# Optimization experiments

Measured on AMD Instinct MI355X. Metric: run time of the kernel, lower is better.

The kernel has to match this reference:

```python
import jax, jax.numpy as jnp
import numpy as np

B, T, P, D, H, L, C = 32, 50000, 100, 512, 16, 6, 256
SCALES = [1, 2, 4]
NS = len(SCALES)
HS = H // NS          # heads per scale = 5
KD = D // H           # key_dim = 32
N = T // P            # num_patches = 500
FF = 4 * D
EPS = 1e-3            # keras LayerNormalization default epsilon


def layernorm(x, g, b):
    m = jnp.mean(x, axis=-1, keepdims=True)
    v = jnp.var(x, axis=-1, keepdims=True)
    return (x - m) * jax.lax.rsqrt(v + EPS) * g + b


def mha(x, Wq, bq, Wk, bk, Wv, bv, Wo, bo):
    # keras MultiHeadAttention: self-attention, scale 1/sqrt(key_dim), biases on
    q = jnp.einsum('bnd,dhk->bnhk', x, Wq) + bq
    k = jnp.einsum('bnd,dhk->bnhk', x, Wk) + bk
    v = jnp.einsum('bnd,dhk->bnhk', x, Wv) + bv
    scores = jnp.einsum('bnhk,bmhk->bhnm', q, k) / jnp.sqrt(jnp.asarray(KD, x.dtype))
    p = jax.nn.softmax(scores, axis=-1)
    o = jnp.einsum('bhnm,bmhk->bnhk', p, v)
    return jnp.einsum('bnhk,hkd->bnd', o, Wo) + bo


def forward(inputs, ln_in_g, ln_in_b, patch_W, patch_b, pos_emb,
            Wq, bq, Wk, bk, Wv, bv, Wo, bo, Wc, bc,
            ln1_g, ln1_b, W1, b1, W2, b2, ln2_g, ln2_b, head_W, head_b):
    x = inputs[..., None]                       # (B, T, 1)
    x = layernorm(x, ln_in_g, ln_in_b)          # degenerate size-1 LN (faithful)
    patches = x.reshape(B, N, P)                # (B, N, P)
    h = patches @ patch_W + patch_b + pos_emb   # (B, N, D)
    for l in range(L):
        outs = []
        for si, s in enumerate(SCALES):
            if s > 1:
                pooled = h.reshape(B, N // s, s, D).mean(axis=2)  # SAME avg_pool1d (N % s == 0)
            else:
                pooled = h
            a = mha(pooled, Wq[l, si], bq[l, si], Wk[l, si], bk[l, si],
                    Wv[l, si], bv[l, si], Wo[l, si], bo[l, si])
            if s > 1:
                a = jnp.repeat(a, s, axis=1)[:, :N]
            outs.append(a)
        comb = jnp.concatenate(outs, axis=-1) @ Wc[l] + bc[l]
        h = h + comb
        h = layernorm(h, ln1_g[l], ln1_b[l])
        f = jax.nn.gelu(h @ W1[l] + b1[l], approximate=False)
        f = f @ W2[l] + b2[l]
        h = h + f
        h = layernorm(h, ln2_g[l], ln2_b[l])
        # Dropout(0.1) identity at inference
    g = h.mean(axis=1)                          # GlobalAveragePooling1D
    return jax.nn.softmax(g @ head_W + head_b, axis=-1)  # key head


def setup_inputs() -> dict:
    key = jax.random.key(0)
    ks = jax.random.split(key, 20)
    r = lambda k, sh, s=0.02: (jax.random.normal(k, sh, jnp.float32) * s)
    f32 = jnp.float32
    return {
        'inputs': jax.random.normal(ks[0], (B, T), f32),
        'ln_in_g': jnp.ones((1,), f32),
        'ln_in_b': r(ks[1], (1,)),
        'patch_W': r(ks[2], (P, D)),
        'patch_b': r(ks[3], (D,)),
        'pos_emb': r(ks[4], (1, N, D)),
        'Wq': r(ks[5], (L, NS, D, HS, KD)), 'bq': jnp.zeros((L, NS, HS, KD), f32),
        'Wk': r(ks[6], (L, NS, D, HS, KD)), 'bk': jnp.zeros((L, NS, HS, KD), f32),
        'Wv': r(ks[7], (L, NS, D, HS, KD)), 'bv': jnp.zeros((L, NS, HS, KD), f32),
        'Wo': r(ks[8], (L, NS, HS, KD, D)), 'bo': jnp.zeros((L, NS, D), f32),
        'Wc': r(ks[9], (L, NS * D, D)), 'bc': jnp.zeros((L, D), f32),
        'ln1_g': jnp.ones((L, D), f32), 'ln1_b': jnp.zeros((L, D), f32),
        'W1': r(ks[10], (L, D, FF)), 'b1': jnp.zeros((L, FF), f32),
        'W2': r(ks[11], (L, FF, D)), 'b2': jnp.zeros((L, D), f32),
        'ln2_g': jnp.ones((L, D), f32), 'ln2_b': jnp.zeros((L, D), f32),
        'head_W': r(ks[12], (D, C)), 'head_b': jnp.zeros((C,), f32),
    }


def reference(inputs, ln_in_g, ln_in_b, patch_W, patch_b, pos_emb,
              Wq, bq, Wk, bk, Wv, bv, Wo, bo, Wc, bc,
              ln1_g, ln1_b, W1, b1, W2, b2, ln2_g, ln2_b, head_W, head_b):
    return forward(inputs, ln_in_g, ln_in_b, patch_W, patch_b, pos_emb,
                   Wq, bq, Wk, bk, Wv, bv, Wo, bo, Wc, bc,
                   ln1_g, ln1_b, W1, b1, W2, b2, ln2_g, ln2_b, head_W, head_b)
```

## Files before the change

kernel.cpp:

```cpp
#include <hip/hip_runtime.h>
#include <math.h>


#define DD 512
#define NN 500
#define HSC 5
#define KDD 32
#define QKVN 160
#define QKV3 480
#define FF 2048
#define NL 6
#define NC 256
#define NB 32
#define LNEPS 1e-3f
#define BM 128
#define BN 64
#define KCHB 64

#define AOFF1 256000
#define AOFF2 384000
#define RTOT 875
#define OSZ 140000
#define MLSZ 4384

typedef __attribute__((ext_vector_type(8))) short bf16x8;
typedef __attribute__((ext_vector_type(4))) float f32x4;

__device__ __forceinline__ float gelu_exact(float x) {
    return 0.5f * x * (1.0f + erff(x * 0.70710678118654752f));
}

__device__ __forceinline__ unsigned int pkbf(float a, float b) {
    unsigned int r;
    asm("v_cvt_pk_bf16_f32 %0, %1, %2" : "=v"(r) : "v"(a), "v"(b));
    return r;
}


template<int POOL, int GATHER>
__device__ __forceinline__ void mstage(
        const float* __restrict__ A, int lda,
        const float* __restrict__ Bcol, int ldb,
        int M, int bm, int k0,
        int ar4, int akq, int bkq,
        float4 (&aR)[2][4], float4 (&bR)[4]) {
    #pragma unroll
    for (int p = 0; p < 2; ++p) {
        int row = min(bm + ar4 + p * 64, M - 1);
        const float* ap;
        if (!GATHER) {
            ap = A + (size_t)row * POOL * lda + k0 + akq;
        } else {
            int si = k0 >> 9;
            ap = A + (si == 0 ? 0 : (si == 1 ? AOFF1 : AOFF2))
               + (size_t)(row >> si) * DD + (k0 & (DD - 1)) + akq;
        }
        #pragma unroll
        for (int i = 0; i < 4; ++i) {
            float4 v = *(const float4*)(ap + i * 4);
            #pragma unroll
            for (int t = 1; t < POOL; ++t) {
                float4 u = *(const float4*)(ap + i * 4 + (size_t)t * lda);
                v.x += u.x; v.y += u.y; v.z += u.z; v.w += u.w;
            }
            if (POOL > 1) {
                const float ip = 1.0f / (float)POOL;
                v.x *= ip; v.y *= ip; v.z *= ip; v.w *= ip;
            }
            aR[p][i] = v;
        }
    }
    #pragma unroll
    for (int i = 0; i < 4; ++i)
        bR[i] = *(const float4*)(Bcol + (size_t)(k0 + bkq + i) * ldb);
}

template<int POOL, int GATHER>
__device__ __forceinline__ void mfma_core(
        const float* __restrict__ A, int lda,
        const float* __restrict__ Bcol, int ldb,
        int M, int bm, int ks, int kend, f32x4 (&acc)[4][2]) {
    __shared__ __align__(16) unsigned short As[128 * 64];
    __shared__ __align__(16) unsigned short Bs[64 * 64];
    const int tid = threadIdx.x;
    const int ar4 = tid >> 2, akq = (tid & 3) * 16;
    const int bkq = (tid >> 4) * 4, bn4 = tid & 15;
    const int lane = tid & 63, wid = tid >> 6;
    const int wm = wid >> 1, wn = wid & 1;

    float4 aR[2][4], bR[4];
    const int nch = (kend - ks) / KCHB;
    mstage<POOL, GATHER>(A, lda, Bcol, ldb, M, bm, ks, ar4, akq, bkq, aR, bR);
    __builtin_amdgcn_sched_barrier(0);

    for (int c = 0; c < nch; ++c) {
        __syncthreads();
        #pragma unroll
        for (int p = 0; p < 2; ++p) {
            int r = ar4 + p * 64;
            int swz = (r & 7) << 4;
            char* base = (char*)As + r * 128;
            #pragma unroll
            for (int i = 0; i < 4; ++i) {
                int cb = (akq + i * 4) * 2;
                *(uint2*)(base + (cb ^ swz)) = make_uint2(
                    pkbf(aR[p][i].x, aR[p][i].y), pkbf(aR[p][i].z, aR[p][i].w));
            }
        }
        {
            const float* b0 = (const float*)&bR[0];
            const float* b1 = (const float*)&bR[1];
            const float* b2 = (const float*)&bR[2];
            const float* b3 = (const float*)&bR[3];
            #pragma unroll
            for (int j = 0; j < 4; ++j) {
                int nrow = bn4 * 4 + j;
                char* base = (char*)Bs + nrow * 128;
                *(uint2*)(base + ((bkq * 2) ^ ((nrow & 7) << 4))) = make_uint2(
                    pkbf(b0[j], b1[j]), pkbf(b2[j], b3[j]));
            }
        }
        __syncthreads();
        if (c + 1 < nch)
            mstage<POOL, GATHER>(A, lda, Bcol, ldb, M, bm,
                                 ks + (c + 1) * KCHB, ar4, akq, bkq, aR, bR);
        __builtin_amdgcn_sched_barrier(0);
        #pragma unroll
        for (int half = 0; half < 2; ++half) {
            const int kb = (half * 32 + (lane >> 4) * 8) * 2;
            bf16x8 af[4], bf[2];
            #pragma unroll
            for (int m = 0; m < 4; ++m) {
                int r = wm * 64 + m * 16 + (lane & 15);
                af[m] = *(const bf16x8*)((const char*)As + r * 128 + (kb ^ ((r & 7) << 4)));
            }
            #pragma unroll
            for (int n = 0; n < 2; ++n) {
                int r = wn * 32 + n * 16 + (lane & 15);
                bf[n] = *(const bf16x8*)((const char*)Bs + r * 128 + (kb ^ ((r & 7) << 4)));
            }
            #pragma unroll
            for (int m = 0; m < 4; ++m)
                #pragma unroll
                for (int n = 0; n < 2; ++n)
                    acc[m][n] = __builtin_amdgcn_mfma_f32_16x16x32_bf16(
                        af[m], bf[n], acc[m][n], 0, 0, 0);
        }
    }
}

#define MACC_INIT(acc) { _Pragma("unroll") for (int m_ = 0; m_ < 4; ++m_) \
    _Pragma("unroll") for (int n_ = 0; n_ < 2; ++n_) \
    _Pragma("unroll") for (int j_ = 0; j_ < 4; ++j_) acc[m_][n_][j_] = 0.f; }

__global__ void colsum_kernel(const float* __restrict__ pw, float* __restrict__ csum) {
    int d = blockIdx.x * blockDim.x + threadIdx.x;
    if (d < DD) {
        float s = 0.f;
        for (int p = 0; p < 100; ++p) s += pw[p * DD + d];
        csum[d] = s;
    }
}

__global__ void init_h(const float* __restrict__ csum, const float* __restrict__ pb,
                       const float* __restrict__ pos, const float* __restrict__ lnb,
                       float* __restrict__ h) {
    int idx = blockIdx.x * 256 + threadIdx.x;
    if (idx >= NN * DD) return;
    int d = idx & (DD - 1);
    h[idx] = lnb[0] * csum[d] + pb[d] + pos[idx];
}

__global__ __launch_bounds__(256, 2) void qkv_part(
        const float* __restrict__ h,
        const float* __restrict__ Wq, const float* __restrict__ Wk,
        const float* __restrict__ Wv,
        float* __restrict__ part, int l) {
    int scale = blockIdx.z >> 1, sp = blockIdx.z & 1;
    int n = NN >> scale;
    int bm = blockIdx.y * BM;
    if (bm >= n) return;
    int bn = blockIdx.x * BN;
    size_t w = (size_t)(l * 3 + scale);
    int tid = threadIdx.x;
    int col = min(bn + (tid & 15) * 4, QKV3 - 4);
    int which = (col >= 320) ? 2 : ((col >= 160) ? 1 : 0);
    const float* Wsel = (which == 0) ? Wq : ((which == 1) ? Wk : Wv);
    const float* Bcol = Wsel + w * DD * QKVN + (col - which * QKVN);
    float* outb = part + (size_t)sp * 420000
                + (scale == 0 ? 0 : (scale == 1 ? 240000 : 360000));

    f32x4 acc[4][2];
    MACC_INIT(acc);
    if (scale == 0)
        mfma_core<1, 0>(h, DD, Bcol, QKVN, n, bm, sp * 256, sp * 256 + 256, acc);
    else if (scale == 1)
        mfma_core<2, 0>(h, DD, Bcol, QKVN, n, bm, sp * 256, sp * 256 + 256, acc);
    else
        mfma_core<4, 0>(h, DD, Bcol, QKVN, n, bm, sp * 256, sp * 256 + 256, acc);

    int lane = tid & 63, wid = tid >> 6, wm = wid >> 1, wn = wid & 1;
    #pragma unroll
    for (int q = 0; q < 2; ++q) {
        int cb = bn + wn * 32 + q * 16;
        if (cb >= QKV3) continue;
        int c2 = cb + (lane & 15);
        #pragma unroll
        for (int m = 0; m < 4; ++m) {
            int r0 = bm + wm * 64 + m * 16 + ((lane >> 4) << 2);
            #pragma unroll
            for (int j = 0; j < 4; ++j) {
                int r = r0 + j;
                if (r < n) outb[(size_t)r * QKV3 + c2] = acc[m][q][j];
            }
        }
    }
}

__global__ void qkv_reduce(const float* __restrict__ part,
                           const float* __restrict__ bq,
                           const float* __restrict__ bk,
                           const float* __restrict__ bv,
                           float* __restrict__ qkvAll, int l) {
    int idx = blockIdx.x * 256 + threadIdx.x;
    if (idx >= 420000) return;
    int scale, base;
    if (idx < 240000) { scale = 0; base = 0; }
    else if (idx < 360000) { scale = 1; base = 240000; }
    else { scale = 2; base = 360000; }
    int rowrem = (idx - base) % QKV3;
    int which = rowrem / QKVN;
    int col = rowrem - which * QKVN;
    float v = part[idx] + part[420000 + idx];
    v += ((which == 0) ? bq : (which == 1 ? bk : bv))[(size_t)(l * 3 + scale) * QKVN + col];
    qkvAll[idx] = v;
}

__global__ __launch_bounds__(256, 2) void attn_split(
        const float* __restrict__ qkvAll, float* __restrict__ oPart,
        float* __restrict__ mPart, float* __restrict__ lPart) {
    int z = blockIdx.z;
    int scale, sp;
    if (z < 4)      { scale = 0; sp = z; }
    else if (z < 6) { scale = 1; sp = z - 4; }
    else            { scale = 2; sp = 0; }
    int n = NN >> scale;
    int qt = blockIdx.x;
    if (qt * 64 >= n) return;
    int hh = blockIdx.y;
    int ks = sp * 128;
    int ke = min(n, ks + 128);
    const float* qkv = qkvAll + (scale == 0 ? 0 : (scale == 1 ? 240000 : 360000));
    int rowb = (scale == 0 ? 0 : (scale == 1 ? 500 : 750));

    int tid = threadIdx.x;
    int kg = tid & 7, qq = tid >> 3;
    int q0 = qt * 64 + qq, q1 = q0 + 32;
    bool ok0 = q0 < n, ok1 = q1 < n;

    float qa[32], qb[32];
    {
        const float* p0 = qkv + (size_t)(ok0 ? q0 : 0) * QKV3 + hh * KDD;
        const float* p1 = qkv + (size_t)(ok1 ? q1 : 0) * QKV3 + hh * KDD;
        #pragma unroll
        for (int c4 = 0; c4 < 8; ++c4) {
            float4 v0 = *(const float4*)(p0 + c4 * 4);
            float4 v1 = *(const float4*)(p1 + c4 * 4);
            qa[c4 * 4] = v0.x; qa[c4 * 4 + 1] = v0.y; qa[c4 * 4 + 2] = v0.z; qa[c4 * 4 + 3] = v0.w;
            qb[c4 * 4] = v1.x; qb[c4 * 4 + 1] = v1.y; qb[c4 * 4 + 2] = v1.z; qb[c4 * 4 + 3] = v1.w;
        }
    }

    __shared__ float Ks[64][36];
    __shared__ float Vs[64][36];
    float o0[32], o1[32];
    #pragma unroll
    for (int c = 0; c < 32; ++c) { o0[c] = 0.f; o1[c] = 0.f; }
    float m0 = -1e30f, m1 = -1e30f, l0 = 0.f, l1 = 0.f;

    int srow = tid >> 2, scol = tid & 3;

    for (int kc = ks; kc < ke; kc += 64) {
        __syncthreads();
        int krow = kc + srow;
        bool ok = krow < ke;
        const float* kp = qkv + (size_t)(ok ? krow : 0) * QKV3 + QKVN + hh * KDD;
        #pragma unroll
        for (int half = 0; half < 2; ++half) {
            int cc = (half * 4 + scol) * 4;
            float4 kv = ok ? *(const float4*)(kp + cc) : make_float4(0.f, 0.f, 0.f, 0.f);
            float4 vv = ok ? *(const float4*)(kp + QKVN + cc) : make_float4(0.f, 0.f, 0.f, 0.f);
            Ks[srow][cc] = kv.x; Ks[srow][cc + 1] = kv.y; Ks[srow][cc + 2] = kv.z; Ks[srow][cc + 3] = kv.w;
            Vs[srow][cc] = vv.x; Vs[srow][cc + 1] = vv.y; Vs[srow][cc + 2] = vv.z; Vs[srow][cc + 3] = vv.w;
        }
        __syncthreads();

        float p0[8], p1[8];
        float cm = -1e30f;
        #pragma unroll
        for (int jj = 0; jj < 8; ++jj) {
            int j = jj * 8 + kg;
            float s0 = 0.f, s1 = 0.f;
            #pragma unroll
            for (int c4 = 0; c4 < 8; ++c4) {
                float4 kv = *(const float4*)&Ks[j][c4 * 4];
                s0 += qa[c4 * 4] * kv.x + qa[c4 * 4 + 1] * kv.y
                    + qa[c4 * 4 + 2] * kv.z + qa[c4 * 4 + 3] * kv.w;
                s1 += qb[c4 * 4] * kv.x + qb[c4 * 4 + 1] * kv.y
                    + qb[c4 * 4 + 2] * kv.z + qb[c4 * 4 + 3] * kv.w;
            }
            s0 *= 0.17677669529663687f;
            s1 *= 0.17677669529663687f;
            if (kc + j >= ke) { s0 = -1e30f; s1 = -1e30f; }
            p0[jj] = s0; p1[jj] = s1;
            cm = fmaxf(cm, fmaxf(s0, s1));
        }
        cm = fmaxf(cm, __shfl_xor(cm, 1));
        cm = fmaxf(cm, __shfl_xor(cm, 2));
        cm = fmaxf(cm, __shfl_xor(cm, 4));

        float mn0 = fmaxf(m0, cm), mn1 = fmaxf(m1, cm);
        float al0 = expf(m0 - mn0), al1 = expf(m1 - mn1);
        m0 = mn0; m1 = mn1;
        float ls0 = 0.f, ls1 = 0.f;
        #pragma unroll
        for (int jj = 0; jj < 8; ++jj) {
            p0[jj] = expf(p0[jj] - mn0); ls0 += p0[jj];
            p1[jj] = expf(p1[jj] - mn1); ls1 += p1[jj];
        }
        l0 = l0 * al0 + ls0;
        l1 = l1 * al1 + ls1;
        #pragma unroll
        for (int c = 0; c < 32; ++c) { o0[c] *= al0; o1[c] *= al1; }
        #pragma unroll
        for (int jj = 0; jj < 8; ++jj) {
            int j = jj * 8 + kg;
            float w0 = p0[jj], w1 = p1[jj];
            #pragma unroll
            for (int c4 = 0; c4 < 8; ++c4) {
                float4 vv = *(const float4*)&Vs[j][c4 * 4];
                o0[c4 * 4]     += w0 * vv.x; o0[c4 * 4 + 1] += w0 * vv.y;
                o0[c4 * 4 + 2] += w0 * vv.z; o0[c4 * 4 + 3] += w0 * vv.w;
                o1[c4 * 4]     += w1 * vv.x; o1[c4 * 4 + 1] += w1 * vv.y;
                o1[c4 * 4 + 2] += w1 * vv.z; o1[c4 * 4 + 3] += w1 * vv.w;
            }
        }
    }
    #pragma unroll
    for (int st = 1; st < 8; st <<= 1) {
        l0 += __shfl_xor(l0, st);
        l1 += __shfl_xor(l1, st);
        #pragma unroll
        for (int c = 0; c < 32; ++c) {
            o0[c] += __shfl_xor(o0[c], st);
            o1[c] += __shfl_xor(o1[c], st);
        }
    }
    if (kg == 0) {
        float* ob = oPart + (size_t)sp * OSZ;
        if (ok0) {
            int r = rowb + q0;
            float* op = ob + (size_t)r * QKVN + hh * KDD;
            #pragma unroll
            for (int c4 = 0; c4 < 8; ++c4) {
                float4 v; v.x = o0[c4*4]; v.y = o0[c4*4+1]; v.z = o0[c4*4+2]; v.w = o0[c4*4+3];
                *(float4*)(op + c4 * 4) = v;
            }
            mPart[sp * MLSZ + r * HSC + hh] = m0;
            lPart[sp * MLSZ + r * HSC + hh] = l0;
        }
        if (ok1) {
            int r = rowb + q1;
            float* op = ob + (size_t)r * QKVN + hh * KDD;
            #pragma unroll
            for (int c4 = 0; c4 < 8; ++c4) {
                float4 v; v.x = o1[c4*4]; v.y = o1[c4*4+1]; v.z = o1[c4*4+2]; v.w = o1[c4*4+3];
                *(float4*)(op + c4 * 4) = v;
            }
            mPart[sp * MLSZ + r * HSC + hh] = m1;
            lPart[sp * MLSZ + r * HSC + hh] = l1;
        }
    }
}

__global__ __launch_bounds__(256, 2) void wo_combine(
        const float* __restrict__ oPart, const float* __restrict__ mPart,
        const float* __restrict__ lPart, const float* __restrict__ Wo,
        const float* __restrict__ bo, float* __restrict__ aAll, int l) {
    int z = blockIdx.z;
    int n = NN >> z;
    int ns = 4 >> z;
    int bm = blockIdx.y * BM;
    if (bm >= n) return;
    int bn = blockIdx.x * BN;
    int rowb = (z == 0 ? 0 : (z == 1 ? 500 : 750));
    size_t w = (size_t)(l * 3 + z);
    int tid = threadIdx.x;
    const float* Bcol = Wo + w * QKVN * DD + bn + (tid & 15) * 4;
    float* C = aAll + (z == 0 ? 0 : (z == 1 ? AOFF1 : AOFF2));

    __shared__ __align__(16) unsigned short As[128 * 64];
    __shared__ __align__(16) unsigned short Bs[64 * 64];
    __shared__ __align__(16) float Wcm[128][24];

    for (int it = tid; it < 128 * HSC; it += 256) {
        int lrow = it / HSC, hh = it - lrow * HSC;
        float w4[4] = {0.f, 0.f, 0.f, 0.f};
        int row = bm + lrow;
        if (row < n) {
            int gr = rowb + row;
            float M = -1e30f;
            for (int s = 0; s < ns; ++s)
                M = fmaxf(M, mPart[s * MLSZ + gr * HSC + hh]);
            float L = 0.f;
            for (int s = 0; s < ns; ++s) {
                float e = expf(mPart[s * MLSZ + gr * HSC + hh] - M);
                w4[s] = e;
                L += e * lPart[s * MLSZ + gr * HSC + hh];
            }
            float inv = 1.f / L;
            for (int s = 0; s < ns; ++s) w4[s] *= inv;
        }
        Wcm[lrow][hh * 4 + 0] = w4[0];
        Wcm[lrow][hh * 4 + 1] = w4[1];
        Wcm[lrow][hh * 4 + 2] = w4[2];
        Wcm[lrow][hh * 4 + 3] = w4[3];
    }
    __syncthreads();

    const int ar4 = tid >> 2, akq = (tid & 3) * 16;
    const int bkq = (tid >> 4) * 4, bn4 = tid & 15;
    const int lane = tid & 63, wid = tid >> 6;
    const int wm = wid >> 1, wn = wid & 1;

    f32x4 acc[4][2];
    MACC_INIT(acc);
    float4 aR[2][4], bR[4];

    auto stage = [&](int k0) {
        int krem = QKVN - k0;
        #pragma unroll
        for (int p = 0; p < 2; ++p) {
            int row = min(bm + ar4 + p * 64, n - 1);
            int lrowc = row - bm;
            #pragma unroll
            for (int i = 0; i < 4; ++i) {
                int kk = akq + i * 4;
                int k = min(k0 + kk, QKVN - 4);
                int hh = min(k >> 5, 4);
                float4 w4 = *(const float4*)&Wcm[lrowc][hh * 4];
                size_t off = (size_t)(rowb + row) * QKVN + k;
                float4 a0 = *(const float4*)(oPart + off);
                float4 v;
                v.x = w4.x * a0.x; v.y = w4.x * a0.y;
                v.z = w4.x * a0.z; v.w = w4.x * a0.w;
                if (ns > 1) {
                    float4 a1 = *(const float4*)(oPart + OSZ + off);
                    v.x += w4.y * a1.x; v.y += w4.y * a1.y;
                    v.z += w4.y * a1.z; v.w += w4.y * a1.w;
                }
                if (ns > 2) {
                    float4 a2 = *(const float4*)(oPart + 2 * OSZ + off);
                    float4 a3 = *(const float4*)(oPart + 3 * OSZ + off);
                    v.x += w4.z * a2.x + w4.w * a3.x;
                    v.y += w4.z * a2.y + w4.w * a3.y;
                    v.z += w4.z * a2.z + w4.w * a3.z;
                    v.w += w4.z * a2.w + w4.w * a3.w;
                }
                bool kv_ = kk < krem;
                v.x = kv_ ? v.x : 0.f; v.y = kv_ ? v.y : 0.f;
                v.z = kv_ ? v.z : 0.f; v.w = kv_ ? v.w : 0.f;
                aR[p][i] = v;
            }
        }
        #pragma unroll
        for (int i = 0; i < 4; ++i) {
            int krow = min(k0 + bkq + i, QKVN - 1);
            bR[i] = *(const float4*)(Bcol + (size_t)krow * DD);
        }
    };

    const int nch = 3;
    stage(0);
    __builtin_amdgcn_sched_barrier(0);
    for (int c = 0; c < nch; ++c) {
        __syncthreads();
        #pragma unroll
        for (int p = 0; p < 2; ++p) {
            int r = ar4 + p * 64;
            int swz = (r & 7) << 4;
            char* base = (char*)As + r * 128;
            #pragma unroll
            for (int i = 0; i < 4; ++i) {
                int cb = (akq + i * 4) * 2;
                *(uint2*)(base + (cb ^ swz)) = make_uint2(
                    pkbf(aR[p][i].x, aR[p][i].y), pkbf(aR[p][i].z, aR[p][i].w));
            }
        }
        {
            const float* b0 = (const float*)&bR[0];
            const float* b1 = (const float*)&bR[1];
            const float* b2 = (const float*)&bR[2];
            const float* b3 = (const float*)&bR[3];
            #pragma unroll
            for (int j = 0; j < 4; ++j) {
                int nrow = bn4 * 4 + j;
                char* base = (char*)Bs + nrow * 128;
                *(uint2*)(base + ((bkq * 2) ^ ((nrow & 7) << 4))) = make_uint2(
                    pkbf(b0[j], b1[j]), pkbf(b2[j], b3[j]));
            }
        }
        __syncthreads();
        if (c + 1 < nch) stage((c + 1) * KCHB);
        __builtin_amdgcn_sched_barrier(0);
        #pragma unroll
        for (int half = 0; half < 2; ++half) {
            const int kb = (half * 32 + (lane >> 4) * 8) * 2;
            bf16x8 af[4], bf[2];
            #pragma unroll
            for (int m = 0; m < 4; ++m) {
                int r = wm * 64 + m * 16 + (lane & 15);
                af[m] = *(const bf16x8*)((const char*)As + r * 128 + (kb ^ ((r & 7) << 4)));
            }
            #pragma unroll
            for (int n2 = 0; n2 < 2; ++n2) {
                int r = wn * 32 + n2 * 16 + (lane & 15);
                bf[n2] = *(const bf16x8*)((const char*)Bs + r * 128 + (kb ^ ((r & 7) << 4)));
            }
            #pragma unroll
            for (int m = 0; m < 4; ++m)
                #pragma unroll
                for (int n2 = 0; n2 < 2; ++n2)
                    acc[m][n2] = __builtin_amdgcn_mfma_f32_16x16x32_bf16(
                        af[m], bf[n2], acc[m][n2], 0, 0, 0);
        }
    }

    const float* bias = bo + w * DD;
    #pragma unroll
    for (int q = 0; q < 2; ++q) {
        int c2 = bn + wn * 32 + q * 16 + (lane & 15);
        float bv_ = bias[c2];
        #pragma unroll
        for (int m = 0; m < 4; ++m) {
            int r0 = bm + wm * 64 + m * 16 + ((lane >> 4) << 2);
            #pragma unroll
            for (int j = 0; j < 4; ++j) {
                int r = r0 + j;
                if (r < n) C[(size_t)r * DD + c2] = acc[m][q][j] + bv_;
            }
        }
    }
}

__global__ __launch_bounds__(256, 2) void comb_part(
        const float* __restrict__ aAll, const float* __restrict__ Wc,
        float* __restrict__ part) {
    int zz = blockIdx.z;
    int bm = blockIdx.y * BM, bn = blockIdx.x * BN;
    int tid = threadIdx.x;
    const float* Bcol = Wc + bn + (tid & 15) * 4;
    f32x4 acc[4][2];
    MACC_INIT(acc);
    mfma_core<1, 1>(aAll, DD, Bcol, DD, NN, bm, zz * 256, zz * 256 + 256, acc);

    float* pz = part + (size_t)zz * NN * DD;
    int lane = tid & 63, wid = tid >> 6, wm = wid >> 1, wn = wid & 1;
    #pragma unroll
    for (int q = 0; q < 2; ++q) {
        int c2 = bn + wn * 32 + q * 16 + (lane & 15);
        #pragma unroll
        for (int m = 0; m < 4; ++m) {
            int r0 = bm + wm * 64 + m * 16 + ((lane >> 4) << 2);
            #pragma unroll
            for (int j = 0; j < 4; ++j) {
                int r = r0 + j;
                if (r < NN) pz[(size_t)r * DD + c2] = acc[m][q][j];
            }
        }
    }
}

__global__ __launch_bounds__(256, 2) void w1_part(
        const float* __restrict__ h, const float* __restrict__ W1,
        float* __restrict__ part) {
    int sp = blockIdx.z;
    int bm = blockIdx.y * BM, bn = blockIdx.x * BN;
    int tid = threadIdx.x;
    const float* Bcol = W1 + bn + (tid & 15) * 4;
    f32x4 acc[4][2];
    MACC_INIT(acc);
    mfma_core<1, 0>(h, DD, Bcol, FF, NN, bm, sp * 256, sp * 256 + 256, acc);

    float* pz = part + (size_t)sp * NN * FF;
    int lane = tid & 63, wid = tid >> 6, wm = wid >> 1, wn = wid & 1;
    #pragma unroll
    for (int q = 0; q < 2; ++q) {
        int c2 = bn + wn * 32 + q * 16 + (lane & 15);
        #pragma unroll
        for (int m = 0; m < 4; ++m) {
            int r0 = bm + wm * 64 + m * 16 + ((lane >> 4) << 2);
            #pragma unroll
            for (int j = 0; j < 4; ++j) {
                int r = r0 + j;
                if (r < NN) pz[(size_t)r * FF + c2] = acc[m][q][j];
            }
        }
    }
}

__global__ void w1_reduce(const float* __restrict__ part,
                          const float* __restrict__ b1, float* __restrict__ f) {
    int idx = blockIdx.x * 256 + threadIdx.x;
    if (idx >= NN * FF) return;
    f[idx] = gelu_exact(part[idx] + part[NN * FF + idx] + b1[idx & (FF - 1)]);
}

__global__ __launch_bounds__(256, 2) void w2_part(
        const float* __restrict__ f, const float* __restrict__ W2,
        float* __restrict__ part) {
    int sp = blockIdx.z;
    int bm = blockIdx.y * BM, bn = blockIdx.x * BN;
    int tid = threadIdx.x;
    const float* Bcol = W2 + bn + (tid & 15) * 4;
    f32x4 acc[4][2];
    MACC_INIT(acc);
    mfma_core<1, 0>(f, FF, Bcol, DD, NN, bm, sp * 256, sp * 256 + 256, acc);

    float* pz = part + (size_t)sp * NN * DD;
    int lane = tid & 63, wid = tid >> 6, wm = wid >> 1, wn = wid & 1;
    #pragma unroll
    for (int q = 0; q < 2; ++q) {
        int c2 = bn + wn * 32 + q * 16 + (lane & 15);
        #pragma unroll
        for (int m = 0; m < 4; ++m) {
            int r0 = bm + wm * 64 + m * 16 + ((lane >> 4) << 2);
            #pragma unroll
            for (int j = 0; j < 4; ++j) {
                int r = r0 + j;
                if (r < NN) pz[(size_t)r * DD + c2] = acc[m][q][j];
            }
        }
    }
}

__global__ void reduce_add_ln(const float* __restrict__ part, int S,
                              const float* __restrict__ bias,
                              float* __restrict__ h,
                              const float* __restrict__ gw,
                              const float* __restrict__ bw) {
    int row = blockIdx.x, t = threadIdx.x;
    size_t idx = (size_t)row * DD + t;
    float x = h[idx] + bias[t];
    for (int s = 0; s < S; ++s) x += part[(size_t)s * NN * DD + idx];
    int lane = t & 63, wv = t >> 6;
    __shared__ float s1[8], s2[8];
    __shared__ float mb[2];
    float sum = x, sq = x * x;
    for (int off = 32; off; off >>= 1) {
        sum += __shfl_down(sum, off);
        sq  += __shfl_down(sq,  off);
    }
    if (lane == 0) { s1[wv] = sum; s2[wv] = sq; }
    __syncthreads();
    if (t == 0) {
        float a = 0.f, b = 0.f;
        for (int i = 0; i < 8; ++i) { a += s1[i]; b += s2[i]; }
        float mean = a / (float)DD;
        float var = b / (float)DD - mean * mean;
        mb[0] = mean;
        mb[1] = rsqrtf(var + LNEPS);
    }
    __syncthreads();
    h[idx] = (x - mb[0]) * mb[1] * gw[t] + bw[t];
}

__global__ void col_mean_part(const float* __restrict__ h, float* __restrict__ partial) {
    int col = blockIdx.x * 256 + threadIdx.x;
    int r0 = blockIdx.y * 20;
    float s = 0.f;
    #pragma unroll
    for (int r = 0; r < 20; ++r) s += h[(size_t)(r0 + r) * DD + col];
    partial[(size_t)blockIdx.y * DD + col] = s;
}

__global__ void head_kernel(const float* __restrict__ partial,
                            const float* __restrict__ hw,
                            const float* __restrict__ hb, float* __restrict__ out) {
    __shared__ float gs[DD];
    __shared__ float r[4];
    __shared__ float bmx, bsum;
    int t = threadIdx.x;
    for (int d = t; d < DD; d += 256) {
        float s = 0.f;
        #pragma unroll
        for (int p = 0; p < 25; ++p) s += partial[(size_t)p * DD + d];
        gs[d] = s / (float)NN;
    }
    __syncthreads();
    float acc = hb[t];
    #pragma unroll 16
    for (int d = 0; d < DD; ++d) acc += gs[d] * hw[(size_t)d * NC + t];
    int lane = t & 63, wv = t >> 6;
    float mx = acc;
    for (int off = 32; off; off >>= 1) mx = fmaxf(mx, __shfl_down(mx, off));
    if (lane == 0) r[wv] = mx;
    __syncthreads();
    if (t == 0) bmx = fmaxf(fmaxf(r[0], r[1]), fmaxf(r[2], r[3]));
    __syncthreads();
    float e = expf(acc - bmx);
    float s = e;
    for (int off = 32; off; off >>= 1) s += __shfl_down(s, off);
    if (lane == 0) r[wv] = s;
    __syncthreads();
    if (t == 0) bsum = 1.f / (r[0] + r[1] + r[2] + r[3]);
    __syncthreads();
    float pv = e * bsum;
    for (int b = 0; b < NB; ++b) out[(size_t)b * NC + t] = pv;
}

extern "C" void kernel_launch(void* const* d_in, const int* in_sizes, int n_in,
                              void* d_out, int out_size, void* d_ws, size_t ws_size,
                              hipStream_t stream) {
    const float* ln_in_b = (const float*)d_in[2];
    const float* patch_W = (const float*)d_in[3];
    const float* patch_b = (const float*)d_in[4];
    const float* pos_emb = (const float*)d_in[5];
    const float* Wq = (const float*)d_in[6];
    const float* bq = (const float*)d_in[7];
    const float* Wk = (const float*)d_in[8];
    const float* bk = (const float*)d_in[9];
    const float* Wv = (const float*)d_in[10];
    const float* bv = (const float*)d_in[11];
    const float* Wo = (const float*)d_in[12];
    const float* bo = (const float*)d_in[13];
    const float* Wc = (const float*)d_in[14];
    const float* bc = (const float*)d_in[15];
    const float* ln1_g = (const float*)d_in[16];
    const float* ln1_b = (const float*)d_in[17];
    const float* W1 = (const float*)d_in[18];
    const float* b1 = (const float*)d_in[19];
    const float* W2 = (const float*)d_in[20];
    const float* b2 = (const float*)d_in[21];
    const float* ln2_g = (const float*)d_in[22];
    const float* ln2_b = (const float*)d_in[23];
    const float* head_W = (const float*)d_in[24];
    const float* head_b = (const float*)d_in[25];
    float* out = (float*)d_out;

    float* ws = (float*)d_ws;
    float* h      = ws;
    float* csum   = h + 256000;
    float* qkvAll = csum + 1024;
    float* oAll   = qkvAll + 420000;
    float* aAll   = oAll + 140000;
    float* f      = aAll + 448000;
    float* part   = f + 1024000;
    float* headp  = part + 2048000;
    float* oPart  = f;
    float* mPart  = f + 560000;
    float* lPart  = mPart + 4 * MLSZ;
    float* qkvP   = part;

    colsum_kernel<<<1, 512, 0, stream>>>(patch_W, csum);
    init_h<<<(NN * DD + 255) / 256, 256, 0, stream>>>(csum, patch_b, pos_emb, ln_in_b, h);

    for (int l = 0; l < NL; ++l) {
        qkv_part<<<dim3(8, 4, 6), 256, 0, stream>>>(h, Wq, Wk, Wv, qkvP, l);
        qkv_reduce<<<(420000 + 255) / 256, 256, 0, stream>>>(qkvP, bq, bk, bv, qkvAll, l);
        attn_split<<<dim3(8, HSC, 7), 256, 0, stream>>>(qkvAll, oPart, mPart, lPart);
        wo_combine<<<dim3(8, 4, 3), 256, 0, stream>>>(oPart, mPart, lPart,
                                                      Wo, bo, aAll, l);
        comb_part<<<dim3(8, 4, 6), 256, 0, stream>>>(
            aAll, Wc + (size_t)l * 3 * DD * DD, part);
        reduce_add_ln<<<NN, DD, 0, stream>>>(part, 6, bc + (size_t)l * DD, h,
                                             ln1_g + (size_t)l * DD, ln1_b + (size_t)l * DD);
        w1_part<<<dim3(32, 4, 2), 256, 0, stream>>>(
            h, W1 + (size_t)l * DD * FF, part);
        w1_reduce<<<(NN * FF + 255) / 256, 256, 0, stream>>>(
            part, b1 + (size_t)l * FF, f);
        w2_part<<<dim3(8, 4, 8), 256, 0, stream>>>(f, W2 + (size_t)l * FF * DD, part);
        reduce_add_ln<<<NN, DD, 0, stream>>>(part, 8, b2 + (size_t)l * DD, h,
                                             ln2_g + (size_t)l * DD, ln2_b + (size_t)l * DD);
    }
    col_mean_part<<<dim3(2, 25), 256, 0, stream>>>(h, headp);
    head_kernel<<<1, 256, 0, stream>>>(headp, head_W, head_b, out);
}
```

Measured before the change: 863.8 us.

## Double split-K factor across GEMMs and fold QKV reduction into attention

Each GEMM's K range per block is halved from 256 to 128, doubling the split-K partition count and grid size for qkv, comb, w1 and w2, with the downstream reduce kernels summing more partials. The separate qkv_reduce kernel is removed; attention now sums the four QKV partials and adds the biases while loading Q/K/V. It also drops the scheduling barriers around the prefetch and adds a tail-masking template path that no caller enables. The goal is better CU occupancy and one less launch, at the cost of more partial-sum memory traffic and redundant K/V partial reads inside attention.

Result: slower. 1.024 ms (+18.5%).

```diff
diff --git a/kernel.cpp b/kernel.cpp
--- a/kernel.cpp
+++ b/kernel.cpp
@@ -22,6 +22,7 @@
 #define RTOT 875
 #define OSZ 140000
 #define MLSZ 4384
+#define QSP 420000
 
 typedef __attribute__((ext_vector_type(8))) short bf16x8;
 typedef __attribute__((ext_vector_type(4))) float f32x4;
@@ -36,12 +37,16 @@
     return r;
 }
 
-
-template<int POOL, int GATHER>
+__device__ __forceinline__ float4 f4add(float4 a, float4 b) {
+    return make_float4(a.x + b.x, a.y + b.y, a.z + b.z, a.w + b.w);
+}
+
+
+template<int POOL, int GATHER, int TAIL>
 __device__ __forceinline__ void mstage(
         const float* __restrict__ A, int lda,
         const float* __restrict__ Bcol, int ldb,
-        int M, int bm, int k0,
+        int M, int bm, int k0, int klim,
         int ar4, int akq, int bkq,
         float4 (&aR)[2][4], float4 (&bR)[4]) {
     #pragma unroll
@@ -49,37 +54,46 @@
         int row = min(bm + ar4 + p * 64, M - 1);
         const float* ap;
         if (!GATHER) {
-            ap = A + (size_t)row * POOL * lda + k0 + akq;
+            ap = A + (size_t)row * POOL * lda;
         } else {
             int si = k0 >> 9;
             ap = A + (si == 0 ? 0 : (si == 1 ? AOFF1 : AOFF2))
-               + (size_t)(row >> si) * DD + (k0 & (DD - 1)) + akq;
+               + (size_t)(row >> si) * DD - (size_t)(k0 & ~(DD - 1));
         }
         #pragma unroll
         for (int i = 0; i < 4; ++i) {
-            float4 v = *(const float4*)(ap + i * 4);
+            int kk = akq + i * 4;
+            int kg = TAIL ? min(k0 + kk, klim - 4) : (k0 + kk);
+            float4 v = *(const float4*)(ap + kg);
             #pragma unroll
             for (int t = 1; t < POOL; ++t) {
-                float4 u = *(const float4*)(ap + i * 4 + (size_t)t * lda);
+                float4 u = *(const float4*)(ap + kg + (size_t)t * lda);
                 v.x += u.x; v.y += u.y; v.z += u.z; v.w += u.w;
             }
             if (POOL > 1) {
                 const float ip = 1.0f / (float)POOL;
                 v.x *= ip; v.y *= ip; v.z *= ip; v.w *= ip;
             }
+            if (TAIL) {
+                bool ok = (k0 + kk) < klim;
+                v.x = ok ? v.x : 0.f; v.y = ok ? v.y : 0.f;
+                v.z = ok ? v.z : 0.f; v.w = ok ? v.w : 0.f;
+            }
             aR[p][i] = v;
         }
     }
     #pragma unroll
-    for (int i = 0; i < 4; ++i)
-        bR[i] = *(const float4*)(Bcol + (size_t)(k0 + bkq + i) * ldb);
-}
-
-template<int POOL, int GATHER>
+    for (int i = 0; i < 4; ++i) {
+        int kr = TAIL ? min(k0 + bkq + i, klim - 1) : (k0 + bkq + i);
+        bR[i] = *(const float4*)(Bcol + (size_t)kr * ldb);
+    }
+}
+
+template<int POOL, int GATHER, int TAIL>
 __device__ __forceinline__ void mfma_core(
         const float* __restrict__ A, int lda,
         const float* __restrict__ Bcol, int ldb,
-        int M, int bm, int ks, int kend, f32x4 (&acc)[4][2]) {
+        int M, int bm, int ks, int nch, int klim, f32x4 (&acc)[4][2]) {
     __shared__ __align__(16) unsigned short As[128 * 64];
     __shared__ __align__(16) unsigned short Bs[64 * 64];
     const int tid = threadIdx.x;
@@ -89,9 +103,8 @@
     const int wm = wid >> 1, wn = wid & 1;
 
     float4 aR[2][4], bR[4];
-    const int nch = (kend - ks) / KCHB;
-    mstage<POOL, GATHER>(A, lda, Bcol, ldb, M, bm, ks, ar4, akq, bkq, aR, bR);
-    __builtin_amdgcn_sched_barrier(0);
+    mstage<POOL, GATHER, TAIL>(A, lda, Bcol, ldb, M, bm, ks, klim,
+                               ar4, akq, bkq, aR, bR);
 
     for (int c = 0; c < nch; ++c) {
         __syncthreads();
@@ -122,9 +135,9 @@
         }
         __syncthreads();
         if (c + 1 < nch)
-            mstage<POOL, GATHER>(A, lda, Bcol, ldb, M, bm,
-                                 ks + (c + 1) * KCHB, ar4, akq, bkq, aR, bR);
-        __builtin_amdgcn_sched_barrier(0);
+            mstage<POOL, GATHER, TAIL>(A, lda, Bcol, ldb, M, bm,
+                                       ks + (c + 1) * KCHB, klim,
+                                       ar4, akq, bkq, aR, bR);
         #pragma unroll
         for (int half = 0; half < 2; ++half) {
             const int kb = (half * 32 + (lane >> 4) * 8) * 2;
@@ -176,7 +189,7 @@
         const float* __restrict__ Wq, const float* __restrict__ Wk,
         const float* __restrict__ Wv,
         float* __restrict__ part, int l) {
-    int scale = blockIdx.z >> 1, sp = blockIdx.z & 1;
+    int scale = blockIdx.z >> 2, ps = blockIdx.z & 3;
     int n = NN >> scale;
     int bm = blockIdx.y * BM;
     if (bm >= n) return;
@@ -187,17 +200,17 @@
     int which = (col >= 320) ? 2 : ((col >= 160) ? 1 : 0);
     const float* Wsel = (which == 0) ? Wq : ((which == 1) ? Wk : Wv);
     const float* Bcol = Wsel + w * DD * QKVN + (col - which * QKVN);
-    float* outb = part + (size_t)sp * 420000
+    float* outb = part + (size_t)ps * QSP
                 + (scale == 0 ? 0 : (scale == 1 ? 240000 : 360000));
 
     f32x4 acc[4][2];
     MACC_INIT(acc);
     if (scale == 0)
-        mfma_core<1, 0>(h, DD, Bcol, QKVN, n, bm, sp * 256, sp * 256 + 256, acc);
+        mfma_core<1, 0, 0>(h, DD, Bcol, QKVN, n, bm, ps * 128, 2, DD, acc);
     else if (scale == 1)
-        mfma_core<2, 0>(h, DD, Bcol, QKVN, n, bm, sp * 256, sp * 256 + 256, acc);
+        mfma_core<2, 0, 0>(h, DD, Bcol, QKVN, n, bm, ps * 128, 2, DD, acc);
     else
-        mfma_core<4, 0>(h, DD, Bcol, QKVN, n, bm, sp * 256, sp * 256 + 256, acc);
+        mfma_core<4, 0, 0>(h, DD, Bcol, QKVN, n, bm, ps * 128, 2, DD, acc);
 
     int lane = tid & 63, wid = tid >> 6, wm = wid >> 1, wn = wid & 1;
     #pragma unroll
@@ -217,28 +230,12 @@
     }
 }
 
-__global__ void qkv_reduce(const float* __restrict__ part,
-                           const float* __restrict__ bq,
-                           const float* __restrict__ bk,
-                           const float* __restrict__ bv,
-                           float* __restrict__ qkvAll, int l) {
-    int idx = blockIdx.x * 256 + threadIdx.x;
-    if (idx >= 420000) return;
-    int scale, base;
-    if (idx < 240000) { scale = 0; base = 0; }
-    else if (idx < 360000) { scale = 1; base = 240000; }
-    else { scale = 2; base = 360000; }
-    int rowrem = (idx - base) % QKV3;
-    int which = rowrem / QKVN;
-    int col = rowrem - which * QKVN;
-    float v = part[idx] + part[420000 + idx];
-    v += ((which == 0) ? bq : (which == 1 ? bk : bv))[(size_t)(l * 3 + scale) * QKVN + col];
-    qkvAll[idx] = v;
-}
-
 __global__ __launch_bounds__(256, 2) void attn_split(
-        const float* __restrict__ qkvAll, float* __restrict__ oPart,
-        float* __restrict__ mPart, float* __restrict__ lPart) {
+        const float* __restrict__ qkvP,
+        const float* __restrict__ bq, const float* __restrict__ bk,
+        const float* __restrict__ bv,
+        float* __restrict__ oPart,
+        float* __restrict__ mPart, float* __restrict__ lPart, int l) {
     int z = blockIdx.z;
     int scale, sp;
     if (z < 4)      { scale = 0; sp = z; }
@@ -250,22 +247,37 @@
     int hh = blockIdx.y;
     int ks = sp * 128;
     int ke = min(n, ks + 128);
-    const float* qkv = qkvAll + (scale == 0 ? 0 : (scale == 1 ? 240000 : 360000));
+    const float* qkv = qkvP + (scale == 0 ? 0 : (scale == 1 ? 240000 : 360000));
     int rowb = (scale == 0 ? 0 : (scale == 1 ? 500 : 750));
+    size_t wb = (size_t)(l * 3 + scale) * QKVN + hh * KDD;
 
     int tid = threadIdx.x;
     int kg = tid & 7, qq = tid >> 3;
     int q0 = qt * 64 + qq, q1 = q0 + 32;
     bool ok0 = q0 < n, ok1 = q1 < n;
 
+    __shared__ float bQs[32], bKs[32], bVs[32];
+    if (tid < 32) bQs[tid] = bq[wb + tid];
+    else if (tid < 64) bKs[tid - 32] = bk[wb + tid - 32];
+    else if (tid < 96) bVs[tid - 64] = bv[wb + tid - 64];
+    __syncthreads();
+
     float qa[32], qb[32];
     {
         const float* p0 = qkv + (size_t)(ok0 ? q0 : 0) * QKV3 + hh * KDD;
         const float* p1 = qkv + (size_t)(ok1 ? q1 : 0) * QKV3 + hh * KDD;
         #pragma unroll
         for (int c4 = 0; c4 < 8; ++c4) {
-            float4 v0 = *(const float4*)(p0 + c4 * 4);
-            float4 v1 = *(const float4*)(p1 + c4 * 4);
+            float4 b4 = *(const float4*)&bQs[c4 * 4];
+            float4 v0 = f4add(f4add(*(const float4*)(p0 + c4 * 4),
+                                    *(const float4*)(p0 + QSP + c4 * 4)),
+                              f4add(*(const float4*)(p0 + 2 * QSP + c4 * 4),
+                                    *(const float4*)(p0 + 3 * QSP + c4 * 4)));
+            float4 v1 = f4add(f4add(*(const float4*)(p1 + c4 * 4),
+                                    *(const float4*)(p1 + QSP + c4 * 4)),
+                              f4add(*(const float4*)(p1 + 2 * QSP + c4 * 4),
+                                    *(const float4*)(p1 + 3 * QSP + c4 * 4)));
+            v0 = f4add(v0, b4); v1 = f4add(v1, b4);
             qa[c4 * 4] = v0.x; qa[c4 * 4 + 1] = v0.y; qa[c4 * 4 + 2] = v0.z; qa[c4 * 4 + 3] = v0.w;
             qb[c4 * 4] = v1.x; qb[c4 * 4 + 1] = v1.y; qb[c4 * 4 + 2] = v1.z; qb[c4 * 4 + 3] = v1.w;
         }
@@ -288,8 +300,18 @@
         #pragma unroll
         for (int half = 0; half < 2; ++half) {
             int cc = (half * 4 + scol) * 4;
-            float4 kv = ok ? *(const float4*)(kp + cc) : make_float4(0.f, 0.f, 0.f, 0.f);
-            float4 vv = ok ? *(const float4*)(kp + QKVN + cc) : make_float4(0.f, 0.f, 0.f, 0.f);
+            float4 kv = f4add(f4add(*(const float4*)(kp + cc),
+                                    *(const float4*)(kp + QSP + cc)),
+                              f4add(*(const float4*)(kp + 2 * QSP + cc),
+                                    *(const float4*)(kp + 3 * QSP + cc)));
+            float4 vv = f4add(f4add(*(const float4*)(kp + QKVN + cc),
+                                    *(const float4*)(kp + QKVN + QSP + cc)),
+                              f4add(*(const float4*)(kp + QKVN + 2 * QSP + cc),
+                                    *(const float4*)(kp + QKVN + 3 * QSP + cc)));
+            kv = f4add(kv, *(const float4*)&bKs[cc]);
+            vv = f4add(vv, *(const float4*)&bVs[cc]);
+            if (!ok) { kv = make_float4(0.f, 0.f, 0.f, 0.f);
+                       vv = make_float4(0.f, 0.f, 0.f, 0.f); }
             Ks[srow][cc] = kv.x; Ks[srow][cc + 1] = kv.y; Ks[srow][cc + 2] = kv.z; Ks[srow][cc + 3] = kv.w;
             Vs[srow][cc] = vv.x; Vs[srow][cc + 1] = vv.y; Vs[srow][cc + 2] = vv.z; Vs[srow][cc + 3] = vv.w;
         }
@@ -482,7 +504,6 @@
 
     const int nch = 3;
     stage(0);
-    __builtin_amdgcn_sched_barrier(0);
     for (int c = 0; c < nch; ++c) {
         __syncthreads();
         #pragma unroll
@@ -512,7 +533,6 @@
         }
         __syncthreads();
         if (c + 1 < nch) stage((c + 1) * KCHB);
-        __builtin_amdgcn_sched_barrier(0);
         #pragma unroll
         for (int half = 0; half < 2; ++half) {
             const int kb = (half * 32 + (lane >> 4) * 8) * 2;
@@ -562,7 +582,7 @@
     const float* Bcol = Wc + bn + (tid & 15) * 4;
     f32x4 acc[4][2];
     MACC_INIT(acc);
-    mfma_core<1, 1>(aAll, DD, Bcol, DD, NN, bm, zz * 256, zz * 256 + 256, acc);
+    mfma_core<1, 1, 0>(aAll, DD, Bcol, DD, NN, bm, zz * 128, 2, 1536, acc);
 
     float* pz = part + (size_t)zz * NN * DD;
     int lane = tid & 63, wid = tid >> 6, wm = wid >> 1, wn = wid & 1;
@@ -590,7 +610,7 @@
     const float* Bcol = W1 + bn + (tid & 15) * 4;
     f32x4 acc[4][2];
     MACC_INIT(acc);
-    mfma_core<1, 0>(h, DD, Bcol, FF, NN, bm, sp * 256, sp * 256 + 256, acc);
+    mfma_core<1, 0, 0>(h, DD, Bcol, FF, NN, bm, sp * 128, 2, DD, acc);
 
     float* pz = part + (size_t)sp * NN * FF;
     int lane = tid & 63, wid = tid >> 6, wm = wid >> 1, wn = wid & 1;
@@ -613,7 +633,9 @@
                           const float* __restrict__ b1, float* __restrict__ f) {
     int idx = blockIdx.x * 256 + threadIdx.x;
     if (idx >= NN * FF) return;
-    f[idx] = gelu_exact(part[idx] + part[NN * FF + idx] + b1[idx & (FF - 1)]);
+    float v = part[idx] + part[NN * FF + idx]
+            + part[2 * NN * FF + idx] + part[3 * NN * FF + idx];
+    f[idx] = gelu_exact(v + b1[idx & (FF - 1)]);
 }
 
 __global__ __launch_bounds__(256, 2) void w2_part(
@@ -625,7 +647,7 @@
     const float* Bcol = W2 + bn + (tid & 15) * 4;
     f32x4 acc[4][2];
     MACC_INIT(acc);
-    mfma_core<1, 0>(f, FF, Bcol, DD, NN, bm, sp * 256, sp * 256 + 256, acc);
+    mfma_core<1, 0, 0>(f, FF, Bcol, DD, NN, bm, sp * 128, 2, FF, acc);
 
     float* pz = part + (size_t)sp * NN * DD;
     int lane = tid & 63, wid = tid >> 6, wm = wid >> 1, wn = wid & 1;
@@ -756,7 +778,7 @@
     float* aAll   = oAll + 140000;
     float* f      = aAll + 448000;
     float* part   = f + 1024000;
-    float* headp  = part + 2048000;
+    float* headp  = part + 4194304;
     float* oPart  = f;
     float* mPart  = f + 560000;
     float* lPart  = mPart + 4 * MLSZ;
@@ -766,21 +788,21 @@
     init_h<<<(NN * DD + 255) / 256, 256, 0, stream>>>(csum, patch_b, pos_emb, ln_in_b, h);
 
     for (int l = 0; l < NL; ++l) {
-        qkv_part<<<dim3(8, 4, 6), 256, 0, stream>>>(h, Wq, Wk, Wv, qkvP, l);
-        qkv_reduce<<<(420000 + 255) / 256, 256, 0, stream>>>(qkvP, bq, bk, bv, qkvAll, l);
-        attn_split<<<dim3(8, HSC, 7), 256, 0, stream>>>(qkvAll, oPart, mPart, lPart);
+        qkv_part<<<dim3(8, 4, 12), 256, 0, stream>>>(h, Wq, Wk, Wv, qkvP, l);
+        attn_split<<<dim3(8, HSC, 7), 256, 0, stream>>>(qkvP, bq, bk, bv,
+                                                        oPart, mPart, lPart, l);
         wo_combine<<<dim3(8, 4, 3), 256, 0, stream>>>(oPart, mPart, lPart,
                                                       Wo, bo, aAll, l);
-        comb_part<<<dim3(8, 4, 6), 256, 0, stream>>>(
+        comb_part<<<dim3(8, 4, 12), 256, 0, stream>>>(
             aAll, Wc + (size_t)l * 3 * DD * DD, part);
-        reduce_add_ln<<<NN, DD, 0, stream>>>(part, 6, bc + (size_t)l * DD, h,
+        reduce_add_ln<<<NN, DD, 0, stream>>>(part, 12, bc + (size_t)l * DD, h,
                                              ln1_g + (size_t)l * DD, ln1_b + (size_t)l * DD);
-        w1_part<<<dim3(32, 4, 2), 256, 0, stream>>>(
+        w1_part<<<dim3(32, 4, 4), 256, 0, stream>>>(
             h, W1 + (size_t)l * DD * FF, part);
         w1_reduce<<<(NN * FF + 255) / 256, 256, 0, stream>>>(
             part, b1 + (size_t)l * FF, f);
-        w2_part<<<dim3(8, 4, 8), 256, 0, stream>>>(f, W2 + (size_t)l * FF * DD, part);
-        reduce_add_ln<<<NN, DD, 0, stream>>>(part, 8, b2 + (size_t)l * DD, h,
+        w2_part<<<dim3(8, 4, 16), 256, 0, stream>>>(f, W2 + (size_t)l * FF * DD, part);
+        reduce_add_ln<<<NN, DD, 0, stream>>>(part, 16, b2 + (size_t)l * DD, h,
                                              ln2_g + (size_t)l * DD, ln2_b + (size_t)l * DD);
     }
     col_mean_part<<<dim3(2, 25), 256, 0, stream>>>(h, headp);
```
